# Kernel tuning notes

Hardware: AMD Instinct MI355X
Metric: run time of the kernel (lower is better)

Reference implementation:

```python
import jax, jax.numpy as jnp
import numpy as np

N_NODES = 100000
N_EDGES = 1000000
N_RELS = 8
N_HEADS = 4
IN_FEAT = 64
OUT_FEAT = 64
D_HEAD = OUT_FEAT // N_HEADS
LEAKY_SLOPE = 0.2


def setup_inputs() -> dict:
    key = jax.random.key(0)
    ks = jax.random.split(key, 8)
    x = jax.random.normal(ks[0], (N_NODES, IN_FEAT), dtype=jnp.float32)
    src_idx = jax.random.randint(ks[1], (N_EDGES,), 0, N_NODES)
    dst_idx = jax.random.randint(ks[2], (N_EDGES,), 0, N_NODES)
    edge_rel = jnp.sort(jax.random.randint(ks[3], (N_EDGES,), 0, N_RELS))
    # xavier-ish small init for weights
    conv_weights = jax.random.normal(ks[4], (N_RELS, N_HEADS, IN_FEAT, D_HEAD), dtype=jnp.float32) * 0.1
    attn_l = jax.random.normal(ks[5], (N_RELS, N_HEADS, D_HEAD), dtype=jnp.float32) * 0.1
    attn_r = jax.random.normal(ks[6], (N_RELS, N_HEADS, D_HEAD), dtype=jnp.float32) * 0.1
    h_bias = jnp.zeros((OUT_FEAT,), dtype=jnp.float32)
    return {
        'x': x, 'src_idx': src_idx, 'dst_idx': dst_idx, 'edge_rel': edge_rel,
        'conv_weights': conv_weights, 'attn_l': attn_l, 'attn_r': attn_r,
        'h_bias': h_bias,
    }


def reference(x, src_idx, dst_idx, edge_rel, conv_weights, attn_l, attn_r, h_bias):
    N = x.shape[0]
    # Per-relation transform of all node features: [R, N, H, D]
    feat_all = jnp.einsum('ni,rhid->rnhd', x, conv_weights)
    # Per-relation attention logits per node: [R, N, H]
    el_all = jnp.einsum('rnhd,rhd->rnh', feat_all, attn_l)
    er_all = jnp.einsum('rnhd,rhd->rnh', feat_all, attn_r)
    # Gather per-edge quantities (relation-specific transform of src/dst)
    feat_e = feat_all[edge_rel, src_idx]          # [E, H, D]
    el = el_all[edge_rel, src_idx]                # [E, H]
    er = er_all[edge_rel, dst_idx]                # [E, H]
    s = jax.nn.leaky_relu(el + er, negative_slope=LEAKY_SLOPE)
    # Edge softmax over incoming edges of each destination node (per head)
    m = jax.ops.segment_max(s, dst_idx, num_segments=N)      # [N, H]
    e = jnp.exp(s - m[dst_idx])                               # [E, H]
    denom = jax.ops.segment_sum(e, dst_idx, num_segments=N)   # [N, H]
    w = e / jnp.maximum(denom[dst_idx], jnp.float32(1e-16))   # [E, H]
    # Weighted aggregation of source features into destination nodes
    agg = jax.ops.segment_sum(feat_e * w[..., None], dst_idx, num_segments=N)  # [N, H, D]
    h = agg.reshape(N, OUT_FEAT) + h_bias
    # activation=None, dropout in eval mode -> identity
    return h
```

## Files before the change

kernel.cpp:

```cpp
#include <hip/hip_runtime.h>
#include <hip/hip_bf16.h>

#define NN 100000
#define NE 1000000
#define NR 8

#define EB 4096
#define NBLK 245
#define NBUCK 196
#define NT (NBUCK*NBLK)
#define NBB 188

#define CAP 256

typedef unsigned short u16;
typedef unsigned int u32;
typedef __attribute__((ext_vector_type(8))) short bf16x8;
typedef __attribute__((ext_vector_type(4))) float f32x4;

static __device__ __forceinline__ float bf2f(u16 u) {
    union { u32 i; float f; } v; v.i = ((u32)u) << 16; return v.f;
}
static __device__ __forceinline__ float bflo(u32 u) {
    union { u32 i; float f; } v; v.i = u << 16; return v.f;
}
static __device__ __forceinline__ float bfhi(u32 u) {
    union { u32 i; float f; } v; v.i = u & 0xffff0000u; return v.f;
}
static __device__ __forceinline__ u16 f2bf(float f) {
    __hip_bfloat16 h = __float2bfloat16(f);
    return *reinterpret_cast<u16*>(&h);
}
static __device__ __forceinline__ float ldf(const void* p, int idx, int isf32) {
    return isf32 ? ((const float*)p)[idx] : bf2f(((const u16*)p)[idx]);
}

static __device__ __forceinline__ int detect_wave(const u16* xw, int lane)
{
    int insane = 0;
    for (int k = lane; k < 512; k += 64) {
        u16 w = xw[k];
        int ex = (w >> 7) & 0xFF;
        bool sane = ((w & 0x7FFF) == 0) || (ex >= 96 && ex <= 159);
        insane += sane ? 0 : 1;
    }
    for (int off = 32; off; off >>= 1) insane += __shfl_down(insane, off);
    return insane;
}

__global__ __launch_bounds__(256) void k_cvt(const void* __restrict__ xin,
                                             u16* __restrict__ xb, int* __restrict__ flag)
{
    __shared__ int sflag;
    int t = threadIdx.x;
    if (t < 64) {
        int insane = detect_wave((const u16*)xin, t);
        if (t == 0) {
            sflag = (insane > 50) ? 1 : 0;
            if (blockIdx.x == 0) *flag = sflag;
        }
    }
    __syncthreads();
    int isf32 = sflag;
    int i = blockIdx.x * 256 + t;
    if (i >= NN * 8) return;
    if (isf32) {
        const float* xf = (const float*)xin;
        u16 o[8];
#pragma unroll
        for (int j = 0; j < 8; ++j) o[j] = f2bf(xf[i * 8 + j]);
        uint4 v;
        v.x = (u32)o[0] | ((u32)o[1] << 16);
        v.y = (u32)o[2] | ((u32)o[3] << 16);
        v.z = (u32)o[4] | ((u32)o[5] << 16);
        v.w = (u32)o[6] | ((u32)o[7] << 16);
        ((uint4*)xb)[i] = v;
    } else {
        ((uint4*)xb)[i] = ((const uint4*)xin)[i];
    }
}

__global__ __launch_bounds__(256) void k0_prep(const void* __restrict__ xin,
                        const void* __restrict__ cw, const void* __restrict__ al,
                        const void* __restrict__ ar, u16* __restrict__ Bpre)
{
    __shared__ int sflag;
    int t = threadIdx.x;
    if (t < 64) {
        int insane = detect_wave((const u16*)xin, t);
        if (t == 0) sflag = (insane > 50) ? 1 : 0;
    }
    __syncthreads();
    int isf32 = sflag;
    int tid = blockIdx.x * 256 + t;
    if (tid >= NR * 5120) return;
    int r = tid / 5120, rem = tid % 5120;
    int c = rem >> 3, j = rem & 7;
    int nt = c >> 7, kk = (c >> 6) & 1, lc = c & 63;
    int i = kk * 32 + ((lc >> 4) << 3) + j;
    int d = lc & 15;
    u16 val;
    if (nt < 4) {
        val = f2bf(ldf(cw, ((r * 4 + nt) * 64 + i) * 16 + d, isf32));
    } else if (d < 8) {
        int h = d >> 1;
        const void* attn = (d & 1) ? ar : al;
        float s = 0.f;
        for (int dd = 0; dd < 16; ++dd)
            s += ldf(cw, ((r * 4 + h) * 64 + i) * 16 + dd, isf32)
               * ldf(attn, (r * 4 + h) * 16 + dd, isf32);
        val = f2bf(s);
    } else {
        val = 0;
    }
    Bpre[tid] = val;
}

__global__ __launch_bounds__(256) void k1_feat(
    const u16* __restrict__ xb, const u16* __restrict__ Bpre,
    u16* __restrict__ feat_all, float* __restrict__ el_all, float* __restrict__ er_all)
{
    __shared__ alignas(16) u16 ldsA[4096];
    __shared__ alignas(16) u16 ldsB[5120];
    int n0 = blockIdx.x * 64;
    int r = blockIdx.y;
    int tid = threadIdx.x;
    int wave = tid >> 6, lane = tid & 63;

    for (int c = tid; c < 512; c += 256) {
        int mt = c >> 7, kk = (c >> 6) & 1, lc = c & 63;
        int node = n0 + mt * 16 + (lc & 15);
        if (node >= NN) node = NN - 1;
        int kbase = kk * 32 + ((lc >> 4) << 3);
        *(uint4*)&ldsA[c * 8] = *(const uint4*)&xb[node * 64 + kbase];
    }
    for (int c = tid; c < 640; c += 256)
        *(uint4*)&ldsB[c * 8] = *(const uint4*)&Bpre[r * 5120 + c * 8];
    __syncthreads();

    bf16x8 afrag0 = *(bf16x8*)&ldsA[((wave * 2 + 0) * 64 + lane) * 8];
    bf16x8 afrag1 = *(bf16x8*)&ldsA[((wave * 2 + 1) * 64 + lane) * 8];
    f32x4 acc[5];
#pragma unroll
    for (int nt = 0; nt < 5; ++nt) acc[nt] = f32x4{0.f, 0.f, 0.f, 0.f};
#pragma unroll
    for (int nt = 0; nt < 5; ++nt) {
        bf16x8 b0 = *(bf16x8*)&ldsB[((nt * 2 + 0) * 64 + lane) * 8];
        bf16x8 b1 = *(bf16x8*)&ldsB[((nt * 2 + 1) * 64 + lane) * 8];
        acc[nt] = __builtin_amdgcn_mfma_f32_16x16x32_bf16(afrag0, b0, acc[nt], 0, 0, 0);
        acc[nt] = __builtin_amdgcn_mfma_f32_16x16x32_bf16(afrag1, b1, acc[nt], 0, 0, 0);
    }

    int col = lane & 15, quad = lane >> 4;
    if (col < 8) {
        int h = col >> 1;
        float* dstp = (col & 1) ? er_all : el_all;
#pragma unroll
        for (int reg = 0; reg < 4; ++reg) {
            int node = n0 + wave * 16 + quad * 4 + reg;
            if (node < NN) dstp[(r * NN + node) * 4 + h] = acc[4][reg];
        }
    }
    __syncthreads();
#pragma unroll
    for (int nt = 0; nt < 4; ++nt) {
        int cg = nt * 16 + col;
#pragma unroll
        for (int reg = 0; reg < 4; ++reg) {
            int row = quad * 4 + reg;
            ldsA[(wave * 16 + row) * 64 + cg] = f2bf(acc[nt][reg]);
        }
    }
    __syncthreads();
    for (int c = tid; c < 512; c += 256) {
        int nl = c >> 3, part = c & 7;
        int node = n0 + nl;
        if (node < NN)
            *(uint4*)&feat_all[(r * NN + node) * 64 + part * 8] = *(uint4*)&ldsA[c * 8];
    }
}

__global__ __launch_bounds__(256) void k_binA(const int* __restrict__ dsti,
                                              int* __restrict__ histT)
{
    __shared__ int hist[NBUCK];
    int t = threadIdx.x, blk = blockIdx.x;
    if (t < NBUCK) hist[t] = 0;
    __syncthreads();
    int base = blk * EB;
    for (int j = 0; j < EB; j += 256) {
        int e = base + j + t;
        if (e < NE) atomicAdd(&hist[dsti[e] >> 9], 1);
    }
    __syncthreads();
    if (t < NBUCK) histT[t * NBLK + blk] = hist[t];
}

__global__ __launch_bounds__(256) void k_scanB1(int* __restrict__ histT,
                                                int* __restrict__ bsum)
{
    __shared__ int wtot[4];
    int t = threadIdx.x;
    int gi = blockIdx.x * 256 + t;
    int v = (gi < NT) ? histT[gi] : 0;
    int lane = t & 63, w = t >> 6;
    int s = v;
#pragma unroll
    for (int m = 1; m < 64; m <<= 1) {
        int u = __shfl_up(s, m);
        if (lane >= m) s += u;
    }
    if (lane == 63) wtot[w] = s;
    __syncthreads();
    int wb = 0;
    for (int i = 0; i < w; ++i) wb += wtot[i];
    if (gi < NT) histT[gi] = wb + s - v;
    if (t == 255) bsum[blockIdx.x] = wb + s;
}

__global__ __launch_bounds__(256) void k_scanB2(const int* __restrict__ bsum,
                                                int* __restrict__ boff)
{
    __shared__ int wtot[4];
    int t = threadIdx.x;
    int v = (t < NBB) ? bsum[t] : 0;
    int lane = t & 63, w = t >> 6;
    int s = v;
#pragma unroll
    for (int m = 1; m < 64; m <<= 1) {
        int u = __shfl_up(s, m);
        if (lane >= m) s += u;
    }
    if (lane == 63) wtot[w] = s;
    __syncthreads();
    int wb = 0;
    for (int i = 0; i < w; ++i) wb += wtot[i];
    if (t < NBB) boff[t] = wb + s - v;
}

__global__ __launch_bounds__(256) void k_scanB3(const int* __restrict__ boff,
                                                int* __restrict__ histT,
                                                int* __restrict__ bstart)
{
    int gi = blockIdx.x * 256 + threadIdx.x;
    if (gi < NT) {
        int val = histT[gi] + boff[blockIdx.x];
        histT[gi] = val;
        if (gi % NBLK == 0) bstart[gi / NBLK] = val;
    }
    if (gi == 0) bstart[NBUCK] = NE;
}

__global__ __launch_bounds__(256) void k_binC(
    const int* __restrict__ srci, const int* __restrict__ dsti,
    const int* __restrict__ reli, const int* __restrict__ histT,
    int* __restrict__ key_b)
{
    __shared__ int cur[NBUCK];
    int t = threadIdx.x, blk = blockIdx.x;
    if (t < NBUCK) cur[t] = histT[t * NBLK + blk];
    __syncthreads();
    int base = blk * EB;
    for (int j = 0; j < EB; j += 256) {
        int e = base + j + t;
        if (e < NE) {
            int d = dsti[e];
            int key = ((d & 511) << 20) | (reli[e] << 17) | srci[e];
            int pos = atomicAdd(&cur[d >> 9], 1);
            key_b[pos] = key;
        }
    }
}

__global__ __launch_bounds__(512) void k_binD(
    const int* __restrict__ bstart, const int* __restrict__ key_b,
    int* __restrict__ key_s, int* __restrict__ off)
{
    __shared__ int cnt[512];
    __shared__ int wtot[8];
    int t = threadIdx.x, b = blockIdx.x;
    int s0 = bstart[b], s1 = bstart[b + 1];
    cnt[t] = 0;
    __syncthreads();
    for (int j = s0 + t; j < s1; j += 512)
        atomicAdd(&cnt[(key_b[j] >> 20) & 511], 1);
    __syncthreads();
    int v = cnt[t];
    int lane = t & 63, w = t >> 6;
    int s = v;
#pragma unroll
    for (int m = 1; m < 64; m <<= 1) {
        int u = __shfl_up(s, m);
        if (lane >= m) s += u;
    }
    if (lane == 63) wtot[w] = s;
    __syncthreads();
    int wb = 0;
    for (int i = 0; i < w; ++i) wb += wtot[i];
    int excl = s0 + wb + s - v;
    int d = (b << 9) + t;
    if (d < NN) off[d] = excl;
    __syncthreads();
    cnt[t] = excl;
    if (b == 0 && t == 0) off[NN] = NE;
    __syncthreads();
    for (int j = s0 + t; j < s1; j += 512) {
        int key = key_b[j];
        int pos = atomicAdd(&cnt[(key >> 20) & 511], 1);
        key_s[pos] = key;
    }
}

__global__ __launch_bounds__(256) void k3_node(
    const int* __restrict__ off, const int* __restrict__ key_s,
    const float* __restrict__ el_all, const float* __restrict__ er_all,
    const u16* __restrict__ feat_all, const void* __restrict__ bias,
    const int* __restrict__ flag, void* __restrict__ out)
{
    __shared__ float ldsER[64][8][4];
    __shared__ int   ldsOffs[65];
    __shared__ int   ldsKey[4][CAP];
    __shared__ float ldsEE[4][CAP][4];
    int t = threadIdx.x;
    int wave = t >> 6, lane = t & 63;
    int eg = lane >> 4;
    int fl = lane & 15;
    int h  = fl >> 2;
    int d0 = blockIdx.x * 64;
    int isf32 = *flag;

#pragma unroll
    for (int r = 0; r < 8; ++r) {
        int dl = t >> 2, q = t & 3;
        int dd = d0 + dl; if (dd >= NN) dd = NN - 1;
        ldsER[dl][r][q] = er_all[(r * NN + dd) * 4 + q];
    }
    if (t < 65) ldsOffs[t] = off[min(d0 + t, NN)];
    __syncthreads();

    int dlo = wave * 16;
    int estart = ldsOffs[dlo], eend = ldsOffs[dlo + 16];
    int count = eend - estart;
    int scount = min(count, CAP);

    for (int j = lane; j < scount; j += 64) {
        int key = key_s[estart + j];
        int rel = (key >> 17) & 7, src = key & 131071;
        int dl = (key >> 20) & 63;
        int kk = rel * NN + src;
        f32x4 el = *(const f32x4*)&el_all[kk * 4];
        f32x4 er = *(const f32x4*)&ldsER[dl][rel][0];
        f32x4 ee;
#pragma unroll
        for (int q = 0; q < 4; ++q) {
            float v = el[q] + er[q];
            v = v > 0.f ? v : 0.2f * v;
            ee[q] = __expf(v);
        }
        ldsKey[wave][j] = kk;
        *(f32x4*)&ldsEE[wave][j][0] = ee;
    }

    float bv0 = ldf(bias, fl * 4 + 0, isf32);
    float bv1 = ldf(bias, fl * 4 + 1, isf32);
    float bv2 = ldf(bias, fl * 4 + 2, isf32);
    float bv3 = ldf(bias, fl * 4 + 3, isf32);

    for (int nl = 0; nl < 16; ++nl) {
        int d = d0 + dlo + nl;
        if (d >= NN) break;
        int s  = ldsOffs[dlo + nl] - estart;
        int e1 = ldsOffs[dlo + nl + 1] - estart;
        float acc0 = 0.f, acc1 = 0.f, acc2 = 0.f, acc3 = 0.f, accW = 0.f;

        int e1c = min(e1, CAP);
        for (int base = s; base < e1c; base += 16) {
            int kk[4]; float w[4];
#pragma unroll
            for (int q = 0; q < 4; ++q) {
                int idx = base + q * 4 + eg;
                bool vld = idx < e1c;
                kk[q] = vld ? ldsKey[wave][idx] : 0;
                w[q]  = vld ? ldsEE[wave][idx][h] : 0.f;
            }
            uint2 u[4];
#pragma unroll
            for (int q = 0; q < 4; ++q)
                u[q] = *(const uint2*)&feat_all[kk[q] * 64 + fl * 4];
#pragma unroll
            for (int q = 0; q < 4; ++q) {
                acc0 += bflo(u[q].x) * w[q];
                acc1 += bfhi(u[q].x) * w[q];
                acc2 += bflo(u[q].y) * w[q];
                acc3 += bfhi(u[q].y) * w[q];
                accW += w[q];
            }
        }
        for (int base = max(s, CAP); base < e1; base += 4) {
            int idx = base + eg;
            int kk0 = 0; float w0 = 0.f;
            if (idx < e1) {
                int key = key_s[estart + idx];
                int rel = (key >> 17) & 7, src = key & 131071;
                kk0 = rel * NN + src;
                int dl = (key >> 20) & 63;
                float v = el_all[kk0 * 4 + h] + ldsER[dl][rel][h];
                v = v > 0.f ? v : 0.2f * v;
                w0 = __expf(v);
            }
            uint2 u = *(const uint2*)&feat_all[kk0 * 64 + fl * 4];
            acc0 += bflo(u.x) * w0;
            acc1 += bfhi(u.x) * w0;
            acc2 += bflo(u.y) * w0;
            acc3 += bfhi(u.y) * w0;
            accW += w0;
        }

#pragma unroll
        for (int m = 16; m < 64; m <<= 1) {
            acc0 += __shfl_xor(acc0, m);
            acc1 += __shfl_xor(acc1, m);
            acc2 += __shfl_xor(acc2, m);
            acc3 += __shfl_xor(acc3, m);
            accW += __shfl_xor(accW, m);
        }
        float invh = 1.f / fmaxf(accW, 1e-16f);
        if (eg == 0) {
            float o0 = acc0 * invh + bv0;
            float o1 = acc1 * invh + bv1;
            float o2 = acc2 * invh + bv2;
            float o3 = acc3 * invh + bv3;
            if (isf32) {
                ((f32x4*)out)[d * 16 + fl] = f32x4{o0, o1, o2, o3};
            } else {
                uint2 st;
                st.x = (u32)f2bf(o0) | ((u32)f2bf(o1) << 16);
                st.y = (u32)f2bf(o2) | ((u32)f2bf(o3) << 16);
                *(uint2*)&((u16*)out)[d * 64 + fl * 4] = st;
            }
        }
    }
}

extern "C" void kernel_launch(void* const* d_in, const int* in_sizes, int n_in,
                              void* d_out, int out_size, void* d_ws, size_t ws_size,
                              hipStream_t stream)
{
    const void* x   = d_in[0];
    const int* srci = (const int*)d_in[1];
    const int* dsti = (const int*)d_in[2];
    const int* reli = (const int*)d_in[3];
    const void* cw  = d_in[4];
    const void* al  = d_in[5];
    const void* ar  = d_in[6];
    const void* hb  = d_in[7];

    char* ws = (char*)d_ws;
    u16*   feat_all = (u16*)  (ws + 0);
    float* el_all   = (float*)(ws + 102400000);
    float* er_all   = (float*)(ws + 115200000);
    int*   key_s    = (int*)  (ws + 128000000);
    int*   key_b    = (int*)  (ws + 132000000);
    int*   off      = (int*)  (ws + 136000000);
    int*   histT    = (int*)  (ws + 136400064);
    int*   bsum     = (int*)  (ws + 136592192);
    int*   boff     = (int*)  (ws + 136592960);
    int*   bstart   = (int*)  (ws + 136593728);
    u16*   Bpre     = (u16*)  (ws + 136594560);
    u16*   xb       = (u16*)  (ws + 136676480);
    int*   flag     = (int*)  (ws + 149476480);

    k_cvt<<<(NN * 8 + 255) / 256, 256, 0, stream>>>(x, xb, flag);
    k0_prep<<<(NR * 5120 + 255) / 256, 256, 0, stream>>>(x, cw, al, ar, Bpre);
    k1_feat<<<dim3((NN + 63) / 64, NR), 256, 0, stream>>>(xb, Bpre, feat_all, el_all, er_all);
    k_binA<<<NBLK, 256, 0, stream>>>(dsti, histT);
    k_scanB1<<<NBB, 256, 0, stream>>>(histT, bsum);
    k_scanB2<<<1, 256, 0, stream>>>(bsum, boff);
    k_scanB3<<<NBB, 256, 0, stream>>>(boff, histT, bstart);
    k_binC<<<NBLK, 256, 0, stream>>>(srci, dsti, reli, histT, key_b);
    k_binD<<<NBUCK, 512, 0, stream>>>(bstart, key_b, key_s, off);
    k3_node<<<(NN + 63) / 64, 256, 0, stream>>>(off, key_s, el_all, er_all, feat_all,
                                                hb, flag, d_out);
}
```

Baseline: 229.9 us.

## Loop relations inside feature kernel, shrink binning blocks, widen binD, drop ER LDS cache

The feature-transform kernel now loops over all 8 relations per block, so the x tile is loaded once and reused instead of once per relation, and it stages output in a separate LDS buffer. The binning passes use smaller edge blocks (more blocks), and the scan and second-level bin kernels use 1024 threads. The node kernel drops its per-block LDS cache of er values and reads er_all directly from global memory per edge. It also lowers the in-LDS edge capacity. These changes trade launch parallelism and LDS use in several places, and the er change adds scattered global reads per edge.

```diff
diff --git a/kernel.cpp b/kernel.cpp
--- a/kernel.cpp
+++ b/kernel.cpp
@@ -5,13 +5,13 @@
 #define NE 1000000
 #define NR 8
 
-#define EB 4096
-#define NBLK 245
+#define EB 1024
+#define NBLK 977
 #define NBUCK 196
 #define NT (NBUCK*NBLK)
-#define NBB 188
-
-#define CAP 256
+#define NBB 749
+
+#define CAP 224
 
 typedef unsigned short u16;
 typedef unsigned int u32;
@@ -122,10 +122,11 @@
 {
     __shared__ alignas(16) u16 ldsA[4096];
     __shared__ alignas(16) u16 ldsB[5120];
+    __shared__ alignas(16) u16 ldsF[4096];
     int n0 = blockIdx.x * 64;
-    int r = blockIdx.y;
     int tid = threadIdx.x;
     int wave = tid >> 6, lane = tid & 63;
+    int col = lane & 15, quad = lane >> 4;
 
     for (int c = tid; c < 512; c += 256) {
         int mt = c >> 7, kk = (c >> 6) & 1, lc = c & 63;
@@ -134,49 +135,51 @@
         int kbase = kk * 32 + ((lc >> 4) << 3);
         *(uint4*)&ldsA[c * 8] = *(const uint4*)&xb[node * 64 + kbase];
     }
-    for (int c = tid; c < 640; c += 256)
-        *(uint4*)&ldsB[c * 8] = *(const uint4*)&Bpre[r * 5120 + c * 8];
-    __syncthreads();
-
+    __syncthreads();
     bf16x8 afrag0 = *(bf16x8*)&ldsA[((wave * 2 + 0) * 64 + lane) * 8];
     bf16x8 afrag1 = *(bf16x8*)&ldsA[((wave * 2 + 1) * 64 + lane) * 8];
-    f32x4 acc[5];
-#pragma unroll
-    for (int nt = 0; nt < 5; ++nt) acc[nt] = f32x4{0.f, 0.f, 0.f, 0.f};
-#pragma unroll
-    for (int nt = 0; nt < 5; ++nt) {
-        bf16x8 b0 = *(bf16x8*)&ldsB[((nt * 2 + 0) * 64 + lane) * 8];
-        bf16x8 b1 = *(bf16x8*)&ldsB[((nt * 2 + 1) * 64 + lane) * 8];
-        acc[nt] = __builtin_amdgcn_mfma_f32_16x16x32_bf16(afrag0, b0, acc[nt], 0, 0, 0);
-        acc[nt] = __builtin_amdgcn_mfma_f32_16x16x32_bf16(afrag1, b1, acc[nt], 0, 0, 0);
-    }
-
-    int col = lane & 15, quad = lane >> 4;
-    if (col < 8) {
-        int h = col >> 1;
-        float* dstp = (col & 1) ? er_all : el_all;
-#pragma unroll
-        for (int reg = 0; reg < 4; ++reg) {
-            int node = n0 + wave * 16 + quad * 4 + reg;
-            if (node < NN) dstp[(r * NN + node) * 4 + h] = acc[4][reg];
-        }
-    }
-    __syncthreads();
-#pragma unroll
-    for (int nt = 0; nt < 4; ++nt) {
-        int cg = nt * 16 + col;
-#pragma unroll
-        for (int reg = 0; reg < 4; ++reg) {
-            int row = quad * 4 + reg;
-            ldsA[(wave * 16 + row) * 64 + cg] = f2bf(acc[nt][reg]);
-        }
-    }
-    __syncthreads();
-    for (int c = tid; c < 512; c += 256) {
-        int nl = c >> 3, part = c & 7;
-        int node = n0 + nl;
-        if (node < NN)
-            *(uint4*)&feat_all[(r * NN + node) * 64 + part * 8] = *(uint4*)&ldsA[c * 8];
+
+    for (int r = 0; r < NR; ++r) {
+        for (int c = tid; c < 640; c += 256)
+            *(uint4*)&ldsB[c * 8] = *(const uint4*)&Bpre[r * 5120 + c * 8];
+        __syncthreads();
+
+        f32x4 acc[5];
+#pragma unroll
+        for (int nt = 0; nt < 5; ++nt) acc[nt] = f32x4{0.f, 0.f, 0.f, 0.f};
+#pragma unroll
+        for (int nt = 0; nt < 5; ++nt) {
+            bf16x8 b0 = *(bf16x8*)&ldsB[((nt * 2 + 0) * 64 + lane) * 8];
+            bf16x8 b1 = *(bf16x8*)&ldsB[((nt * 2 + 1) * 64 + lane) * 8];
+            acc[nt] = __builtin_amdgcn_mfma_f32_16x16x32_bf16(afrag0, b0, acc[nt], 0, 0, 0);
+            acc[nt] = __builtin_amdgcn_mfma_f32_16x16x32_bf16(afrag1, b1, acc[nt], 0, 0, 0);
+        }
+
+        if (col < 8) {
+            int h = col >> 1;
+            float* dstp = (col & 1) ? er_all : el_all;
+#pragma unroll
+            for (int reg = 0; reg < 4; ++reg) {
+                int node = n0 + wave * 16 + quad * 4 + reg;
+                if (node < NN) dstp[(r * NN + node) * 4 + h] = acc[4][reg];
+            }
+        }
+#pragma unroll
+        for (int nt = 0; nt < 4; ++nt) {
+            int cg = nt * 16 + col;
+#pragma unroll
+            for (int reg = 0; reg < 4; ++reg) {
+                int row = quad * 4 + reg;
+                ldsF[(wave * 16 + row) * 64 + cg] = f2bf(acc[nt][reg]);
+            }
+        }
+        __syncthreads();
+        for (int c = tid; c < 512; c += 256) {
+            int nl = c >> 3, part = c & 7;
+            int node = n0 + nl;
+            if (node < NN)
+                *(uint4*)&feat_all[(r * NN + node) * 64 + part * 8] = *(uint4*)&ldsF[c * 8];
+        }
     }
 }
 
@@ -218,10 +221,10 @@
     if (t == 255) bsum[blockIdx.x] = wb + s;
 }
 
-__global__ __launch_bounds__(256) void k_scanB2(const int* __restrict__ bsum,
-                                                int* __restrict__ boff)
-{
-    __shared__ int wtot[4];
+__global__ __launch_bounds__(1024) void k_scanB2(const int* __restrict__ bsum,
+                                                 int* __restrict__ boff)
+{
+    __shared__ int wtot[16];
     int t = threadIdx.x;
     int v = (t < NBB) ? bsum[t] : 0;
     int lane = t & 63, w = t >> 6;
@@ -272,7 +275,7 @@
     }
 }
 
-__global__ __launch_bounds__(512) void k_binD(
+__global__ __launch_bounds__(1024) void k_binD(
     const int* __restrict__ bstart, const int* __restrict__ key_b,
     int* __restrict__ key_s, int* __restrict__ off)
 {
@@ -280,31 +283,36 @@
     __shared__ int wtot[8];
     int t = threadIdx.x, b = blockIdx.x;
     int s0 = bstart[b], s1 = bstart[b + 1];
-    cnt[t] = 0;
-    __syncthreads();
-    for (int j = s0 + t; j < s1; j += 512)
+    if (t < 512) cnt[t] = 0;
+    __syncthreads();
+    for (int j = s0 + t; j < s1; j += 1024)
         atomicAdd(&cnt[(key_b[j] >> 20) & 511], 1);
     __syncthreads();
-    int v = cnt[t];
-    int lane = t & 63, w = t >> 6;
-    int s = v;
-#pragma unroll
-    for (int m = 1; m < 64; m <<= 1) {
-        int u = __shfl_up(s, m);
-        if (lane >= m) s += u;
-    }
-    if (lane == 63) wtot[w] = s;
-    __syncthreads();
-    int wb = 0;
-    for (int i = 0; i < w; ++i) wb += wtot[i];
-    int excl = s0 + wb + s - v;
-    int d = (b << 9) + t;
-    if (d < NN) off[d] = excl;
-    __syncthreads();
-    cnt[t] = excl;
+    int excl = 0;
+    if (t < 512) {
+        int v = cnt[t];
+        int lane = t & 63, w = t >> 6;
+        int s = v;
+#pragma unroll
+        for (int m = 1; m < 64; m <<= 1) {
+            int u = __shfl_up(s, m);
+            if (lane >= m) s += u;
+        }
+        if (lane == 63) wtot[w] = s;
+        __syncthreads();
+        int wb = 0;
+        for (int i = 0; i < w; ++i) wb += wtot[i];
+        excl = s0 + wb + s - v;
+        int d = (b << 9) + t;
+        if (d < NN) off[d] = excl;
+    } else {
+        __syncthreads();
+    }
+    __syncthreads();
+    if (t < 512) cnt[t] = excl;
     if (b == 0 && t == 0) off[NN] = NE;
     __syncthreads();
-    for (int j = s0 + t; j < s1; j += 512) {
+    for (int j = s0 + t; j < s1; j += 1024) {
         int key = key_b[j];
         int pos = atomicAdd(&cnt[(key >> 20) & 511], 1);
         key_s[pos] = key;
@@ -317,7 +325,6 @@
     const u16* __restrict__ feat_all, const void* __restrict__ bias,
     const int* __restrict__ flag, void* __restrict__ out)
 {
-    __shared__ float ldsER[64][8][4];
     __shared__ int   ldsOffs[65];
     __shared__ int   ldsKey[4][CAP];
     __shared__ float ldsEE[4][CAP][4];
@@ -329,12 +336,6 @@
     int d0 = blockIdx.x * 64;
     int isf32 = *flag;
 
-#pragma unroll
-    for (int r = 0; r < 8; ++r) {
-        int dl = t >> 2, q = t & 3;
-        int dd = d0 + dl; if (dd >= NN) dd = NN - 1;
-        ldsER[dl][r][q] = er_all[(r * NN + dd) * 4 + q];
-    }
     if (t < 65) ldsOffs[t] = off[min(d0 + t, NN)];
     __syncthreads();
 
@@ -346,10 +347,10 @@
     for (int j = lane; j < scount; j += 64) {
         int key = key_s[estart + j];
         int rel = (key >> 17) & 7, src = key & 131071;
-        int dl = (key >> 20) & 63;
+        int d = d0 + ((key >> 20) & 63);
         int kk = rel * NN + src;
         f32x4 el = *(const f32x4*)&el_all[kk * 4];
-        f32x4 er = *(const f32x4*)&ldsER[dl][rel][0];
+        f32x4 er = *(const f32x4*)&er_all[(rel * NN + d) * 4];
         f32x4 ee;
 #pragma unroll
         for (int q = 0; q < 4; ++q) {
@@ -403,8 +404,7 @@
                 int key = key_s[estart + idx];
                 int rel = (key >> 17) & 7, src = key & 131071;
                 kk0 = rel * NN + src;
-                int dl = (key >> 20) & 63;
-                float v = el_all[kk0 * 4 + h] + ldsER[dl][rel][h];
+                float v = el_all[kk0 * 4 + h] + er_all[(rel * NN + d) * 4 + h];
                 v = v > 0.f ? v : 0.2f * v;
                 w0 = __expf(v);
             }
@@ -463,22 +463,22 @@
     int*   key_b    = (int*)  (ws + 132000000);
     int*   off      = (int*)  (ws + 136000000);
     int*   histT    = (int*)  (ws + 136400064);
-    int*   bsum     = (int*)  (ws + 136592192);
-    int*   boff     = (int*)  (ws + 136592960);
-    int*   bstart   = (int*)  (ws + 136593728);
-    u16*   Bpre     = (u16*)  (ws + 136594560);
-    u16*   xb       = (u16*)  (ws + 136676480);
-    int*   flag     = (int*)  (ws + 149476480);
+    int*   bsum     = (int*)  (ws + 137166032);
+    int*   boff     = (int*)  (ws + 137169040);
+    int*   bstart   = (int*)  (ws + 137172048);
+    u16*   Bpre     = (u16*)  (ws + 137172880);
+    u16*   xb       = (u16*)  (ws + 137254800);
+    int*   flag     = (int*)  (ws + 150054800);
 
     k_cvt<<<(NN * 8 + 255) / 256, 256, 0, stream>>>(x, xb, flag);
     k0_prep<<<(NR * 5120 + 255) / 256, 256, 0, stream>>>(x, cw, al, ar, Bpre);
-    k1_feat<<<dim3((NN + 63) / 64, NR), 256, 0, stream>>>(xb, Bpre, feat_all, el_all, er_all);
+    k1_feat<<<(NN + 63) / 64, 256, 0, stream>>>(xb, Bpre, feat_all, el_all, er_all);
     k_binA<<<NBLK, 256, 0, stream>>>(dsti, histT);
     k_scanB1<<<NBB, 256, 0, stream>>>(histT, bsum);
-    k_scanB2<<<1, 256, 0, stream>>>(bsum, boff);
+    k_scanB2<<<1, 1024, 0, stream>>>(bsum, boff);
     k_scanB3<<<NBB, 256, 0, stream>>>(boff, histT, bstart);
     k_binC<<<NBLK, 256, 0, stream>>>(srci, dsti, reli, histT, key_b);
-    k_binD<<<NBUCK, 512, 0, stream>>>(bstart, key_b, key_s, off);
+    k_binD<<<NBUCK, 1024, 0, stream>>>(bstart, key_b, key_s, off);
     k3_node<<<(NN + 63) / 64, 256, 0, stream>>>(off, key_s, el_all, er_all, feat_all,
                                                 hb, flag, d_out);
 }
```

Result: faster. 220.6 us (-4.0%).
